# Kernel optimization log

Hardware: AMD Instinct MI355X
Metric: run time of the kernel (lower is better)

## Reference

```python
import jax, jax.numpy as jnp
import numpy as np


def setup_inputs() -> dict:
    key = jax.random.key(0)
    k1, k2, k3 = jax.random.split(key, 3)
    N1, N2, D = 2048, 32768, 1024
    return {
        "query_seq": jax.random.normal(k1, (N1, D), dtype=jnp.float32),
        "matching_set": jax.random.normal(k2, (N2, D), dtype=jnp.float32),
        "synth_set": jax.random.normal(k3, (N2, D), dtype=jnp.float32),
        "topk": 4,
    }


def reference(query_seq, matching_set, synth_set, topk):
    # fast_cosine_dist: the torch code computes dot products via the
    # -cdist^2 + ||a||^2 + ||b||^2 identity; mathematically this is q @ m^T.
    q_norm = jnp.linalg.norm(query_seq, axis=-1)        # [N1]
    m_norm = jnp.linalg.norm(matching_set, axis=-1)     # [N2]
    dotprod = jnp.einsum('nd,md->nm', query_seq, matching_set)  # [N1, N2]
    dists = 1.0 - dotprod / (q_norm[:, None] * m_norm[None, :])
    # topk smallest distances -> top_k of negated dists
    _, idx = jax.lax.top_k(-dists, topk)                # [N1, topk]
    out_feats = synth_set[idx].mean(axis=1)             # [N1, D]
    return out_feats
```

## Files before the change

kernel.cpp:

```cpp
#include <hip/hip_runtime.h>

#define N1 2048
#define N2 32768
#define DD 1024
#define BM 128
#define BN 128
#define BK 128
#define NBN (N2 / BN)
#define NBM (N1 / BM)
#define KT  (DD / BK)

typedef __attribute__((ext_vector_type(8))) int   i32x8;
typedef __attribute__((ext_vector_type(4))) int   i32x4;
typedef __attribute__((ext_vector_type(4))) float f32x4;

typedef const __attribute__((address_space(1))) void gv_t;
typedef __attribute__((address_space(3))) void       lv_t;

__device__ __forceinline__ void gload16(const void* g, void* l) {
  __builtin_amdgcn_global_load_lds((gv_t*)g, (lv_t*)l, 16, 0, 0);
}

__device__ __forceinline__ unsigned ordf(float x) {
  union { float f; unsigned u; } a; a.f = x;
  return a.u ^ ((unsigned)((int)a.u >> 31) | 0x80000000u);
}

__global__ __launch_bounds__(256) void nrmcvt8(const float* __restrict__ src,
                                               unsigned char* __restrict__ dst,
                                               float* __restrict__ invn) {
  const int row = blockIdx.x, t = threadIdx.x;
  const float4* s4 = (const float4*)(src + (size_t)row * DD);
  float4 v = s4[t];
  float ss = v.x * v.x + v.y * v.y + v.z * v.z + v.w * v.w;
  #pragma unroll
  for (int o = 32; o > 0; o >>= 1) ss += __shfl_down(ss, o, 64);
  __shared__ float red[4];
  if ((t & 63) == 0) red[t >> 6] = ss;
  __syncthreads();
  float inv = 1.0f / sqrtf(red[0] + red[1] + red[2] + red[3]);
  float sc = inv * 16.0f;
  int p = 0;
  p = __builtin_amdgcn_cvt_pk_fp8_f32(v.x * sc, v.y * sc, p, false);
  p = __builtin_amdgcn_cvt_pk_fp8_f32(v.z * sc, v.w * sc, p, true);
  ((unsigned*)(dst + (size_t)row * DD))[t] = (unsigned)p;
  if (invn != nullptr && t == 0) invn[row] = inv;
}

__global__ __launch_bounds__(256, 2) void gemm_topk(
    const unsigned char* __restrict__ qb,
    const unsigned char* __restrict__ mbn,
    unsigned* __restrict__ cand_k) {
  __shared__ char lds[65536];
  const int tid  = threadIdx.x;
  const int lane = tid & 63;
  const int w = tid >> 6, wr = w >> 1, wc = w & 1;

  int bid = blockIdx.x;
  int swz = (bid & 7) * (NBM * NBN / 8) + (bid >> 3);
  const int bm = swz >> 8;
  const int bn = swz & (NBN - 1);

  const char* aG = (const char*)(qb  + (size_t)bm * BM * DD);
  const char* bG = (const char*)(mbn + (size_t)bn * BN * DD);

  f32x4 acc[4][4] = {};

  auto stage = [&](int d, int kt) {
    #pragma unroll
    for (int it = 0; it < 4; ++it) {
      int p = it * 256 + tid;
      int r = p >> 3, c = p & 7, cs = c ^ (r & 7);
      gload16(aG + (size_t)r * DD + kt * BK + cs * 16,
              lds + d * 32768 + p * 16);
    }
    #pragma unroll
    for (int it = 0; it < 4; ++it) {
      int p = it * 256 + tid;
      int r = p >> 3, c = p & 7, cs = c ^ (r & 7);
      gload16(bG + (size_t)r * DD + kt * BK + cs * 16,
              lds + d * 32768 + 16384 + p * 16);
    }
  };

  auto compute = [&](int d) {
    const char* Abuf = lds + d * 32768;
    const char* Bbuf = Abuf + 16384;
    const int g2 = 2 * (lane >> 4);
    i32x8 af[4], bb[4];
    #pragma unroll
    for (int i = 0; i < 4; ++i) {
      int ra = wr * 64 + i * 16 + (lane & 15);
      i32x4 lo = *(const i32x4*)(Abuf + ra * 128 + ((g2 ^ (ra & 7)) * 16));
      i32x4 hi = *(const i32x4*)(Abuf + ra * 128 + (((g2 + 1) ^ (ra & 7)) * 16));
      af[i] = __builtin_shufflevector(lo, hi, 0, 1, 2, 3, 4, 5, 6, 7);
      int rb = wc * 64 + i * 16 + (lane & 15);
      i32x4 blo = *(const i32x4*)(Bbuf + rb * 128 + ((g2 ^ (rb & 7)) * 16));
      i32x4 bhi = *(const i32x4*)(Bbuf + rb * 128 + (((g2 + 1) ^ (rb & 7)) * 16));
      bb[i] = __builtin_shufflevector(blo, bhi, 0, 1, 2, 3, 4, 5, 6, 7);
    }
    #pragma unroll
    for (int i = 0; i < 4; ++i)
      #pragma unroll
      for (int j = 0; j < 4; ++j)
        acc[i][j] = __builtin_amdgcn_mfma_scale_f32_16x16x128_f8f6f4(
            af[i], bb[j], acc[i][j], 0 , 0 ,
            0, 0x7F7F7F7F, 0, 0x7F7F7F7F );
  };

  stage(0, 0);
  __syncthreads();
  for (int t = 0; t < KT; ++t) {
    if (t + 1 < KT) stage((t + 1) & 1, t + 1);
    compute(t & 1);
    __syncthreads();
  }

  float* sc = (float*)lds;
  #pragma unroll
  for (int i = 0; i < 4; ++i)
    #pragma unroll
    for (int j = 0; j < 4; ++j)
      #pragma unroll
      for (int q = 0; q < 4; ++q) {
        int r = wr * 64 + i * 16 + (lane >> 4) * 4 + q;
        int c = wc * 64 + j * 16 + (lane & 15);
        sc[r * 128 + ((c + r) & 127)] = acc[i][j][q];
      }
  __syncthreads();

  const int srow = tid >> 1, strip = tid & 1;
  unsigned k0 = 0, k1 = 0, k2 = 0, k3 = 0;
  for (int i = 0; i < 64; ++i) {
    int c = strip * 64 + i;
    float s = sc[srow * 128 + ((c + srow) & 127)];
    unsigned key = (ordf(s) & 0xFFFF8000u) | (unsigned)(bn * BN + c);
    unsigned b = key, t2;
    t2 = k0 < b ? k0 : b; k0 = k0 < b ? b : k0; b = t2;
    t2 = k1 < b ? k1 : b; k1 = k1 < b ? b : k1; b = t2;
    t2 = k2 < b ? k2 : b; k2 = k2 < b ? b : k2; b = t2;
    k3 = k3 < b ? b : k3;
  }
  unsigned* dst = cand_k + (size_t)(bm * BM + srow) * (NBN * 8) + bn * 8 + strip * 4;
  *(uint4*)dst = make_uint4(k0, k1, k2, k3);
}

__global__ __launch_bounds__(256) void finalize(
    const float* __restrict__ q, const float* __restrict__ m,
    const float* __restrict__ synth, const unsigned* __restrict__ cand_k,
    const float* __restrict__ inv_mn, float* __restrict__ out) {
  const int lane = threadIdx.x & 63;
  const int row  = blockIdx.x * 4 + (threadIdx.x >> 6);

  uint4 kk[8];
  const uint4* kp = (const uint4*)(cand_k + (size_t)row * (NBN * 8));
  #pragma unroll
  for (int ii = 0; ii < 8; ++ii) kk[ii] = kp[ii * 64 + lane];

  const float4* qp = (const float4*)(q + (size_t)row * DD);
  float4 qv[4];
  #pragma unroll
  for (int ph = 0; ph < 4; ++ph) qv[ph] = qp[ph * 64 + lane];

  unsigned wk[16];
  #pragma unroll
  for (int it = 0; it < 16; ++it) {
    unsigned lm = 0;
    #pragma unroll
    for (int ii = 0; ii < 8; ++ii) {
      unsigned a = kk[ii].x > kk[ii].y ? kk[ii].x : kk[ii].y;
      unsigned b = kk[ii].z > kk[ii].w ? kk[ii].z : kk[ii].w;
      a = a > b ? a : b;
      lm = lm > a ? lm : a;
    }
    #pragma unroll
    for (int o = 1; o < 64; o <<= 1) {
      unsigned other = (unsigned)__shfl_xor((int)lm, o, 64);
      lm = lm > other ? lm : other;
    }
    wk[it] = lm;
    #pragma unroll
    for (int ii = 0; ii < 8; ++ii) {
      kk[ii].x = kk[ii].x == lm ? 0u : kk[ii].x;
      kk[ii].y = kk[ii].y == lm ? 0u : kk[ii].y;
      kk[ii].z = kk[ii].z == lm ? 0u : kk[ii].z;
      kk[ii].w = kk[ii].w == lm ? 0u : kk[ii].w;
    }
  }

  float cosv[16]; int gidx[16];
  #pragma unroll
  for (int it = 0; it < 16; ++it) {
    int g = (int)(wk[it] & 0x7FFFu);
    gidx[it] = g;
    const float4* mp = (const float4*)(m + (size_t)g * DD);
    float d = 0.f;
    #pragma unroll
    for (int ph = 0; ph < 4; ++ph) {
      float4 mv = mp[ph * 64 + lane];
      d += mv.x * qv[ph].x + mv.y * qv[ph].y + mv.z * qv[ph].z + mv.w * qv[ph].w;
    }
    #pragma unroll
    for (int o = 1; o < 64; o <<= 1) d += __shfl_xor(d, o, 64);
    cosv[it] = d * inv_mn[g];
  }

  int sel[4]; bool used[16] = {};
  #pragma unroll
  for (int s = 0; s < 4; ++s) {
    float bv = -1e30f; int bg = 0x7FFFFFFF; int bj = -1;
    #pragma unroll
    for (int j = 0; j < 16; ++j) {
      bool better = !used[j] && (cosv[j] > bv || (cosv[j] == bv && gidx[j] < bg));
      bv = better ? cosv[j] : bv;
      bg = better ? gidx[j] : bg;
      bj = better ? j : bj;
    }
    sel[s] = bg;
    #pragma unroll
    for (int j = 0; j < 16; ++j) used[j] = used[j] || (j == bj);
  }

  const float4* s0 = (const float4*)(synth + (size_t)sel[0] * DD);
  const float4* s1 = (const float4*)(synth + (size_t)sel[1] * DD);
  const float4* s2 = (const float4*)(synth + (size_t)sel[2] * DD);
  const float4* s3 = (const float4*)(synth + (size_t)sel[3] * DD);
  float4* op = (float4*)(out + (size_t)row * DD);
  #pragma unroll
  for (int ph = 0; ph < 4; ++ph) {
    int ix = ph * 64 + lane;
    float4 a = s0[ix], b = s1[ix], c = s2[ix], d = s3[ix];
    float4 r;
    r.x = (a.x + b.x + c.x + d.x) * 0.25f;
    r.y = (a.y + b.y + c.y + d.y) * 0.25f;
    r.z = (a.z + b.z + c.z + d.z) * 0.25f;
    r.w = (a.w + b.w + c.w + d.w) * 0.25f;
    op[ix] = r;
  }
}

extern "C" void kernel_launch(void* const* d_in, const int* in_sizes, int n_in,
                              void* d_out, int out_size, void* d_ws, size_t ws_size,
                              hipStream_t stream) {
  (void)in_sizes; (void)n_in; (void)out_size; (void)ws_size;
  const float* q = (const float*)d_in[0];
  const float* m = (const float*)d_in[1];
  const float* s = (const float*)d_in[2];
  float* out = (float*)d_out;

  char* w = (char*)d_ws;
  unsigned char* qb     = (unsigned char*)w;
  unsigned char* mb     = (unsigned char*)(w + (2ull << 20));
  float*         inv_mn = (float*)(w + (40ull << 20));
  unsigned*      cand_k = (unsigned*)(w + (41ull << 20));

  nrmcvt8<<<N1, 256, 0, stream>>>(q, qb, nullptr);
  nrmcvt8<<<N2, 256, 0, stream>>>(m, mb, inv_mn);
  gemm_topk<<<NBM * NBN, 256, 0, stream>>>(qb, mb, cand_k);
  finalize<<<N1 / 4, 256, 0, stream>>>(q, m, s, cand_k, inv_mn, out);
}
```

Measured before the change: 176.9 us.

## Load A fragments directly from global into registers, stage only B in LDS

Each wave now reads its query (A) MFMA fragments straight from global memory into registers, double-buffered across K steps, and only the matching-set (B) tile goes through LDS. This halves LDS staging traffic and LDS reads per iteration and removes the A tile from the shared-memory footprint. The cost is that the two column waves duplicate the global A reads, which rely on L2/L1 hits, and the extra register buffers raise register pressure at two blocks per CU. The loop is manually unrolled by two so the register buffers alternate.

```diff
diff --git a/kernel.cpp b/kernel.cpp
--- a/kernel.cpp
+++ b/kernel.cpp
@@ -61,58 +61,62 @@
   const int bm = swz >> 8;
   const int bn = swz & (NBN - 1);
 
-  const char* aG = (const char*)(qb  + (size_t)bm * BM * DD);
   const char* bG = (const char*)(mbn + (size_t)bn * BN * DD);
+  const char* aW = (const char*)(qb +
+      (size_t)(bm * BM + wr * 64 + (lane & 15)) * DD) + (lane >> 4) * 32;
 
   f32x4 acc[4][4] = {};
 
-  auto stage = [&](int d, int kt) {
-    #pragma unroll
-    for (int it = 0; it < 4; ++it) {
-      int p = it * 256 + tid;
-      int r = p >> 3, c = p & 7, cs = c ^ (r & 7);
-      gload16(aG + (size_t)r * DD + kt * BK + cs * 16,
-              lds + d * 32768 + p * 16);
-    }
+  auto stageB = [&](int d, int kt) {
     #pragma unroll
     for (int it = 0; it < 4; ++it) {
       int p = it * 256 + tid;
       int r = p >> 3, c = p & 7, cs = c ^ (r & 7);
       gload16(bG + (size_t)r * DD + kt * BK + cs * 16,
-              lds + d * 32768 + 16384 + p * 16);
+              lds + d * 16384 + p * 16);
     }
   };
 
-  auto compute = [&](int d) {
-    const char* Abuf = lds + d * 32768;
-    const char* Bbuf = Abuf + 16384;
+  i32x4 alo[4], ahi[4], nlo[4], nhi[4];
+  auto loadA = [&](int kt, i32x4 (&lo)[4], i32x4 (&hi)[4]) {
+    #pragma unroll
+    for (int i = 0; i < 4; ++i) {
+      lo[i] = *(const i32x4*)(aW + (size_t)i * 16 * DD + kt * BK);
+      hi[i] = *(const i32x4*)(aW + (size_t)i * 16 * DD + kt * BK + 16);
+    }
+  };
+
+  auto compute = [&](int d, const i32x4 (&lo)[4], const i32x4 (&hi)[4]) {
+    const char* Bbuf = lds + d * 16384;
     const int g2 = 2 * (lane >> 4);
-    i32x8 af[4], bb[4];
+    i32x8 bb[4];
     #pragma unroll
     for (int i = 0; i < 4; ++i) {
-      int ra = wr * 64 + i * 16 + (lane & 15);
-      i32x4 lo = *(const i32x4*)(Abuf + ra * 128 + ((g2 ^ (ra & 7)) * 16));
-      i32x4 hi = *(const i32x4*)(Abuf + ra * 128 + (((g2 + 1) ^ (ra & 7)) * 16));
-      af[i] = __builtin_shufflevector(lo, hi, 0, 1, 2, 3, 4, 5, 6, 7);
       int rb = wc * 64 + i * 16 + (lane & 15);
       i32x4 blo = *(const i32x4*)(Bbuf + rb * 128 + ((g2 ^ (rb & 7)) * 16));
       i32x4 bhi = *(const i32x4*)(Bbuf + rb * 128 + (((g2 + 1) ^ (rb & 7)) * 16));
       bb[i] = __builtin_shufflevector(blo, bhi, 0, 1, 2, 3, 4, 5, 6, 7);
     }
     #pragma unroll
-    for (int i = 0; i < 4; ++i)
+    for (int i = 0; i < 4; ++i) {
+      i32x8 af = __builtin_shufflevector(lo[i], hi[i], 0, 1, 2, 3, 4, 5, 6, 7);
       #pragma unroll
       for (int j = 0; j < 4; ++j)
         acc[i][j] = __builtin_amdgcn_mfma_scale_f32_16x16x128_f8f6f4(
-            af[i], bb[j], acc[i][j], 0 , 0 ,
+            af, bb[j], acc[i][j], 0 , 0 ,
             0, 0x7F7F7F7F, 0, 0x7F7F7F7F );
+    }
   };
 
-  stage(0, 0);
+  stageB(0, 0); loadA(0, alo, ahi);
   __syncthreads();
-  for (int t = 0; t < KT; ++t) {
-    if (t + 1 < KT) stage((t + 1) & 1, t + 1);
-    compute(t & 1);
+  #pragma unroll 1
+  for (int t = 0; t < KT; t += 2) {
+    if (t + 1 < KT) { stageB(1, t + 1); loadA(t + 1, nlo, nhi); }
+    compute(0, alo, ahi);
+    __syncthreads();
+    if (t + 2 < KT) { stageB(0, t + 2); loadA(t + 2, alo, ahi); }
+    compute(1, nlo, nhi);
     __syncthreads();
   }
 
```

Result: slower. 247.9 us (+40.2%).
